# Optimization experiments

Measured on AMD Instinct MI355X. Metric: run time of the kernel, lower is better.

## Reference

```python
import jax, jax.numpy as jnp
import numpy as np

E = 2048   # embed_dim
H = 16     # num_heads
D = E // H # head_dim = 128
ROPE_BASE = 10000.0


def setup_inputs() -> dict:
    key = jax.random.key(0)
    ks = jax.random.split(key, 9)
    s = 0.02
    x = jax.random.normal(ks[0], (2, 2048, E), dtype=jnp.float32)
    Wq = jax.random.normal(ks[1], (E, E), dtype=jnp.float32) * s
    bq = jax.random.normal(ks[2], (E,), dtype=jnp.float32) * s
    Wk = jax.random.normal(ks[3], (E, E), dtype=jnp.float32) * s
    bk = jax.random.normal(ks[4], (E,), dtype=jnp.float32) * s
    Wv = jax.random.normal(ks[5], (E, E), dtype=jnp.float32) * s
    bv = jax.random.normal(ks[6], (E,), dtype=jnp.float32) * s
    Wo = jax.random.normal(ks[7], (E, E), dtype=jnp.float32) * s
    bo = jax.random.normal(ks[8], (E,), dtype=jnp.float32) * s
    return {"x": x, "Wq": Wq, "bq": bq, "Wk": Wk, "bk": bk,
            "Wv": Wv, "bv": bv, "Wo": Wo, "bo": bo}


def _rope_cos_sin(seq_len, dtype):
    inv_freq = 1.0 / (ROPE_BASE ** (jnp.arange(0, D, 2, dtype=jnp.float32) / D))
    pos = jnp.arange(seq_len, dtype=jnp.float32)
    freqs = pos[:, None] * inv_freq[None, :]          # (S, D/2)
    emb = jnp.concatenate([freqs, freqs], axis=-1)    # (S, D)
    return jnp.cos(emb).astype(dtype), jnp.sin(emb).astype(dtype)


def _rotate_half(t):
    t1, t2 = jnp.split(t, 2, axis=-1)
    return jnp.concatenate([-t2, t1], axis=-1)


def reference(x, Wq, bq, Wk, bk, Wv, bv, Wo, bo):
    B, S, _ = x.shape
    # QKV projections (torch Linear: x @ W.T + b)
    q = (x @ Wq.T + bq).reshape(B, S, H, D).transpose(0, 2, 1, 3)  # (B,H,S,D)
    k = (x @ Wk.T + bk).reshape(B, S, H, D).transpose(0, 2, 1, 3)
    v = (x @ Wv.T + bv).reshape(B, S, H, D).transpose(0, 2, 1, 3)
    # RoPE
    cos, sin = _rope_cos_sin(S, x.dtype)              # (S, D) each
    q = q * cos + _rotate_half(q) * sin
    k = k * cos + _rotate_half(k) * sin
    # Causal scaled dot-product attention
    scale = 1.0 / jnp.sqrt(jnp.asarray(D, dtype=x.dtype))
    scores = jnp.einsum('bhqd,bhkd->bhqk', q, k) * scale
    causal = jnp.tril(jnp.ones((S, S), dtype=bool))
    scores = jnp.where(causal, scores, jnp.asarray(-jnp.inf, dtype=x.dtype))
    attn = jax.nn.softmax(scores, axis=-1)
    out = jnp.einsum('bhqk,bhkd->bhqd', attn, v)      # (B,H,S,D)
    out = out.transpose(0, 2, 1, 3).reshape(B, S, E)
    return out @ Wo.T + bo
```

## Files before the change

kernel.cpp:

```cpp
#include <hip/hip_runtime.h>
#include <math.h>

typedef __bf16 bf16;
typedef __attribute__((ext_vector_type(2))) __bf16 bf16x2;
typedef __attribute__((ext_vector_type(4))) __bf16 bf16x4;
typedef __attribute__((ext_vector_type(8))) __bf16 bf16x8;
typedef __attribute__((ext_vector_type(4))) float f32x4;

#define GLD16(g, l) __builtin_amdgcn_global_load_lds( \
    (const __attribute__((address_space(1))) void*)(g), \
    (__attribute__((address_space(3))) void*)(l), 16, 0, 0)


__global__ void cast_bf16_kernel(const float* __restrict__ in, bf16* __restrict__ out, int n4) {
  int i = blockIdx.x * blockDim.x + threadIdx.x;
  if (i >= n4) return;
  float4 f = ((const float4*)in)[i];
  bf16x4 o;
  o[0] = (bf16)f.x; o[1] = (bf16)f.y; o[2] = (bf16)f.z; o[3] = (bf16)f.w;
  ((bf16x4*)out)[i] = o;
}

__global__ void bias_cat_kernel(const float* __restrict__ bq, const float* __restrict__ bk,
                                const float* __restrict__ bv, float* __restrict__ out) {
  int i = blockIdx.x * blockDim.x + threadIdx.x;
  if (i >= 6144) return;
  out[i] = (i < 2048) ? bq[i] : (i < 4096 ? bk[i - 2048] : bv[i - 4096]);
}

__global__ void rope_table_kernel(float* __restrict__ cost, float* __restrict__ sint) {
  int i = blockIdx.x * blockDim.x + threadIdx.x;
  int s = i >> 6, d = i & 63;
  float inv = powf(10000.0f, -(float)d / 64.0f);
  float ang = (float)s * inv;
  cost[i] = cosf(ang);
  sint[i] = sinf(ang);
}

__global__ void rope_transpose_kernel(const bf16* __restrict__ qkv,
                                      const float* __restrict__ cost, const float* __restrict__ sint,
                                      bf16* __restrict__ qr, bf16* __restrict__ kr, bf16* __restrict__ vr) {
  int idx = blockIdx.x * blockDim.x + threadIdx.x;
  int d = idx & 127;
  int h = (idx >> 7) & 15;
  int s = (idx >> 11) & 2047;
  int b = idx >> 22;
  const bf16* row = qkv + (size_t)(b * 2048 + s) * 6144;
  float c  = cost[(s << 6) | (d & 63)];
  float sn = sint[(s << 6) | (d & 63)];
  float qv = (float)row[(h << 7) | d];
  float qp = (float)row[(h << 7) | (d ^ 64)];
  float kv = (float)row[2048 + ((h << 7) | d)];
  float kp = (float)row[2048 + ((h << 7) | (d ^ 64))];
  float vv = (float)row[4096 + ((h << 7) | d)];
  float qrot = (d < 64) ? -qp : qp;
  float krot = (d < 64) ? -kp : kp;
  size_t o = ((size_t)((b << 4) | h) * 2048 + s) * 128 + d;
  qr[o] = (bf16)(qv * c + qrot * sn);
  kr[o] = (bf16)(kv * c + krot * sn);
  vr[o] = (bf16)vv;
}

__global__ void transpose_v_kernel(const bf16* __restrict__ vr, bf16* __restrict__ vt) {
  __shared__ bf16 Vl[64 * 72];
  const int bh = blockIdx.z;
  const int st = blockIdx.y;
  const int dt = blockIdx.x;
  const bf16* src = vr + ((size_t)bh * 2048 + st * 64) * 128 + dt * 64;
  bf16* dst = vt + ((size_t)bh * 128 + dt * 64) * 2048 + st * 64;
  const int t = threadIdx.x;
#pragma unroll
  for (int i = 0; i < 2; ++i) {
    int c = i * 256 + t;
    int r = c >> 3, c0 = (c & 7) * 8;
    *(bf16x8*)&Vl[r * 72 + c0] = *(const bf16x8*)&src[(size_t)r * 128 + c0];
  }
  __syncthreads();
#pragma unroll
  for (int i = 0; i < 2; ++i) {
    int c = i * 256 + t;
    int r = c >> 3, c0 = (c & 7) * 8;
    bf16x8 v;
#pragma unroll
    for (int j = 0; j < 8; ++j) v[j] = Vl[(c0 + j) * 72 + r];
    *(bf16x8*)&dst[(size_t)r * 2048 + c0] = v;
  }
}

template<bool OUT_BF16>
__global__ __launch_bounds__(256)
void gemm_bt_kernel(const bf16* __restrict__ A, const bf16* __restrict__ B,
                    const float* __restrict__ bias, void* __restrict__ Cp,
                    int M, int N, int K) {
  __shared__ bf16 Al[128 * 32];
  __shared__ bf16 Bl[128 * 32];
  const int t = threadIdx.x;
  const int wid = t >> 6, lane = t & 63;
  const int wr = wid >> 1, wc = wid & 1;
  const int lr = lane & 15, lk = lane >> 4;
  const int tm = blockIdx.y, tn = blockIdx.x;
  const bf16* Ab = A + (size_t)tm * 128 * K;
  const bf16* Bb = B + (size_t)tn * 128 * K;
  f32x4 acc[4][4] = {};
  for (int k0 = 0; k0 < K; k0 += 32) {
    __syncthreads();
#pragma unroll
    for (int c = 0; c < 2; ++c) {
      int e = (c * 256 + t) * 8;
      int row = e >> 5, kk = e & 31;
      GLD16(Ab + (size_t)row * K + k0 + kk, &Al[e]);
      GLD16(Bb + (size_t)row * K + k0 + kk, &Bl[e]);
    }
    __syncthreads();
    bf16x8 af[4], bf[4];
#pragma unroll
    for (int m = 0; m < 4; ++m) af[m] = *(const bf16x8*)&Al[(wr * 64 + m * 16 + lr) * 32 + lk * 8];
#pragma unroll
    for (int n = 0; n < 4; ++n) bf[n] = *(const bf16x8*)&Bl[(wc * 64 + n * 16 + lr) * 32 + lk * 8];
#pragma unroll
    for (int m = 0; m < 4; ++m)
#pragma unroll
      for (int n = 0; n < 4; ++n)
        acc[m][n] = __builtin_amdgcn_mfma_f32_16x16x32_bf16(af[m], bf[n], acc[m][n], 0, 0, 0);
  }
  const int rb = tm * 128 + wr * 64, cb = tn * 128 + wc * 64;
#pragma unroll
  for (int n = 0; n < 4; ++n) {
    int col = cb + n * 16 + lr;
    float bvl = bias[col];
#pragma unroll
    for (int m = 0; m < 4; ++m) {
#pragma unroll
      for (int r = 0; r < 4; ++r) {
        int row = rb + m * 16 + lk * 4 + r;
        float v = acc[m][n][r] + bvl;
        if (OUT_BF16) ((bf16*)Cp)[(size_t)row * N + col] = (bf16)v;
        else          ((float*)Cp)[(size_t)row * N + col] = v;
      }
    }
  }
}

template<bool OUT_BF16>
__global__ __launch_bounds__(512, 2)
void gemm256_kernel(const bf16* __restrict__ A, const bf16* __restrict__ B,
                    const float* __restrict__ bias, void* __restrict__ Cp,
                    int M, int N, int K) {
  __shared__ bf16 Al[2][2][128 * 64];
  __shared__ bf16 Bl[2][2][128 * 64];
  const int t = threadIdx.x;
  const int wid = t >> 6, lane = t & 63;
  const int wr = wid >> 2, wc = wid & 3;
  const int lr = lane & 15, lk = lane >> 4;
  const int tm = blockIdx.y, tn = blockIdx.x;
  const bf16* Ab = A + (size_t)tm * 256 * K;
  const bf16* Bb = B + (size_t)tn * 256 * K;
  const int NT = K >> 6;

  auto stageA = [&](int bp, int h, int kt) {
#pragma unroll
    for (int q = 0; q < 2; ++q) {
      int e = q * 512 + t;
      int r = e >> 3, c = e & 7;
      GLD16(Ab + (size_t)(h * 128 + r) * K + kt * 64 + ((c ^ (r & 7)) << 3), &Al[bp][h][e * 8]);
    }
  };
  auto stageB = [&](int bp, int h, int kt) {
#pragma unroll
    for (int q = 0; q < 2; ++q) {
      int e = q * 512 + t;
      int r = e >> 3, c = e & 7;
      GLD16(Bb + (size_t)(h * 128 + r) * K + kt * 64 + ((c ^ (r & 7)) << 3), &Bl[bp][h][e * 8]);
    }
  };

  f32x4 acc[8][4] = {};

  stageB(0, 0, 0); stageB(0, 1, 0);
  stageA(0, 0, 0); stageA(0, 1, 0);
  if (NT > 1) { stageB(1, 0, 1); stageB(1, 1, 1); }
  asm volatile("s_waitcnt vmcnt(4)" ::: "memory");
  __builtin_amdgcn_s_barrier();
  __builtin_amdgcn_sched_barrier(0);

  for (int u = 0; u < NT; ++u) {
    const int p = u & 1;
    const bf16* Ah = Al[p][wr];
    const bf16* Bh = Bl[p][wc >> 1];
    const int rb0 = (wc & 1) * 64;
    bf16x8 bfr[4][2];
#pragma unroll
    for (int j = 0; j < 4; ++j) {
      bf16x8 afr[2][2];
      if (j == 0) {
#pragma unroll
        for (int n = 0; n < 4; ++n)
#pragma unroll
          for (int kk = 0; kk < 2; ++kk) {
            int r = rb0 + n * 16 + lr;
            bfr[n][kk] = *(const bf16x8*)&Bh[r * 64 + ((((kk << 2) | lk) ^ (r & 7)) << 3)];
          }
      }
#pragma unroll
      for (int m2 = 0; m2 < 2; ++m2)
#pragma unroll
        for (int kk = 0; kk < 2; ++kk) {
          int r = (2 * j + m2) * 16 + lr;
          afr[m2][kk] = *(const bf16x8*)&Ah[r * 64 + ((((kk << 2) | lk) ^ (r & 7)) << 3)];
        }
      if (j == 0)      { if (u + 1 < NT) stageA(p ^ 1, 0, u + 1); }
      else if (j == 1) { if (u + 1 < NT) stageA(p ^ 1, 1, u + 1); }
      else if (j == 2) { if (u + 2 < NT) stageB(p, 0, u + 2); }
      else             { if (u + 2 < NT) stageB(p, 1, u + 2); }
      __builtin_amdgcn_s_barrier();
      asm volatile("s_waitcnt lgkmcnt(0)" ::: "memory");
      __builtin_amdgcn_sched_barrier(0);
      __builtin_amdgcn_s_setprio(1);
#pragma unroll
      for (int m2 = 0; m2 < 2; ++m2)
#pragma unroll
        for (int n = 0; n < 4; ++n)
#pragma unroll
          for (int kk = 0; kk < 2; ++kk)
            acc[2 * j + m2][n] = __builtin_amdgcn_mfma_f32_16x16x32_bf16(
                afr[m2][kk], bfr[n][kk], acc[2 * j + m2][n], 0, 0, 0);
      __builtin_amdgcn_s_setprio(0);
      __builtin_amdgcn_sched_barrier(0);
      if (j == 3) {
        if (u + 2 < NT) { asm volatile("s_waitcnt vmcnt(4)" ::: "memory"); }
        else            { asm volatile("s_waitcnt vmcnt(0)" ::: "memory"); }
      }
      __builtin_amdgcn_s_barrier();
      __builtin_amdgcn_sched_barrier(0);
    }
  }

  const int rb = tm * 256 + wr * 128, cb = tn * 256 + wc * 64;
#pragma unroll
  for (int n = 0; n < 4; ++n) {
    int col = cb + n * 16 + lr;
    float bvl = bias[col];
#pragma unroll
    for (int m = 0; m < 8; ++m) {
#pragma unroll
      for (int r = 0; r < 4; ++r) {
        int row = rb + m * 16 + lk * 4 + r;
        float v = acc[m][n][r] + bvl;
        if (OUT_BF16) ((bf16*)Cp)[(size_t)row * N + col] = (bf16)v;
        else          ((float*)Cp)[(size_t)row * N + col] = v;
      }
    }
  }
}

__global__ __launch_bounds__(256, 2)
void attn_kernel(const bf16* __restrict__ Q, const bf16* __restrict__ Kc,
                 const bf16* __restrict__ Vtg, bf16* __restrict__ O, int S) {
  __shared__ bf16 Kl[2][64 * 128];
  __shared__ bf16 Vt[2][128 * 64];
  __shared__ bf16 Pl[4][16 * 64];
  const int t = threadIdx.x, wid = t >> 6, lane = t & 63;
  const int lr = lane & 15, lk = lane >> 4;
  const int bh = blockIdx.y;
  const int NQ = S >> 6;
  const int qtA = blockIdx.x, qtB = NQ - 1 - qtA;
  const int ntA = qtA + 1, ntB = qtB + 1, total = ntA + ntB;
  const bf16* Qb = Q + (size_t)bh * S * 128;
  const bf16* Kb = Kc + (size_t)bh * S * 128;
  const bf16* Vb = Vtg + (size_t)bh * 128 * S;
  const int b = bh >> 4, h = bh & 15;
  const float scale = 0.08838834764831845f;

  bf16x8 qf[4];
  auto loadQ = [&](int q0) {
    int qrow = q0 + wid * 16 + lr;
#pragma unroll
    for (int kb = 0; kb < 4; ++kb)
      qf[kb] = *(const bf16x8*)&Qb[(size_t)qrow * 128 + kb * 32 + lk * 8];
  };
  auto stage = [&](int buf, int kv0) {
#pragma unroll
    for (int c = 0; c < 4; ++c) {
      int fc = c * 256 + t;
      int kvr = fc >> 4, cc = fc & 15;
      GLD16(Kb + (size_t)(kv0 + kvr) * 128 + (cc ^ (kvr & 7)) * 8, &Kl[buf][fc * 8]);
      int dr = fc >> 3, c2 = fc & 7;
      GLD16(Vb + (size_t)dr * S + kv0 + (c2 ^ (dr & 7)) * 8, &Vt[buf][fc * 8]);
    }
  };

  f32x4 o[8] = {};
  float mrun[4], lrun[4];
#pragma unroll
  for (int r = 0; r < 4; ++r) { mrun[r] = -INFINITY; lrun[r] = 0.f; }

  loadQ(qtA * 64);
  stage(0, 0);
  __syncthreads();
  int cur = 0;
  for (int ti = 0; ti < total; ++ti) {
    if (ti + 1 < total) {
      int tn = ti + 1;
      stage(cur ^ 1, ((tn < ntA) ? tn : tn - ntA) * 64);
    }
    __builtin_amdgcn_sched_barrier(0);
    const bool isA = ti < ntA;
    const int tt = isA ? ti : ti - ntA;
    const int nt = isA ? ntA : ntB;
    const int q0 = (isA ? qtA : qtB) * 64;
    const int kv0 = tt * 64;
    f32x4 sa[4];
    __builtin_amdgcn_s_setprio(1);
#pragma unroll
    for (int n = 0; n < 4; ++n) {
      sa[n] = (f32x4){0.f, 0.f, 0.f, 0.f};
      int kvl = n * 16 + lr;
#pragma unroll
      for (int kb = 0; kb < 4; ++kb) {
        bf16x8 kf = *(const bf16x8*)&Kl[cur][kvl * 128 + (((kb << 2) | lk) ^ (kvl & 7)) * 8];
        sa[n] = __builtin_amdgcn_mfma_f32_16x16x32_bf16(qf[kb], kf, sa[n], 0, 0, 0);
      }
    }
    __builtin_amdgcn_s_setprio(0);
    float p[4][4];
    float tmax[4] = {-INFINITY, -INFINITY, -INFINITY, -INFINITY};
    const bool lastTile = (tt == nt - 1);
#pragma unroll
    for (int n = 0; n < 4; ++n)
#pragma unroll
      for (int r = 0; r < 4; ++r) {
        float s = sa[n][r] * scale;
        if (lastTile) {
          int kvg = kv0 + n * 16 + lr;
          int qg = q0 + wid * 16 + lk * 4 + r;
          if (kvg > qg) s = -INFINITY;
        }
        p[n][r] = s;
        tmax[r] = fmaxf(tmax[r], s);
      }
#pragma unroll
    for (int r = 0; r < 4; ++r)
#pragma unroll
      for (int off = 1; off < 16; off <<= 1)
        tmax[r] = fmaxf(tmax[r], __shfl_xor(tmax[r], off));
    float alpha[4], rsum[4];
#pragma unroll
    for (int r = 0; r < 4; ++r) {
      float mnew = fmaxf(mrun[r], tmax[r]);
      alpha[r] = __expf(mrun[r] - mnew);
      mrun[r] = mnew;
      rsum[r] = 0.f;
#pragma unroll
      for (int n = 0; n < 4; ++n) {
        p[n][r] = __expf(p[n][r] - mnew);
        rsum[r] += p[n][r];
      }
    }
#pragma unroll
    for (int r = 0; r < 4; ++r) {
#pragma unroll
      for (int off = 1; off < 16; off <<= 1)
        rsum[r] += __shfl_xor(rsum[r], off);
      lrun[r] = lrun[r] * alpha[r] + rsum[r];
    }
#pragma unroll
    for (int n8 = 0; n8 < 8; ++n8)
#pragma unroll
      for (int r = 0; r < 4; ++r)
        o[n8][r] *= alpha[r];
#pragma unroll
    for (int n = 0; n < 4; ++n)
#pragma unroll
      for (int r = 0; r < 4; ++r) {
        int row = lk * 4 + r, col = n * 16 + lr;
        Pl[wid][(row * 64 + col) ^ ((row & 7) << 3)] = (bf16)p[n][r];
      }
    __builtin_amdgcn_s_setprio(1);
#pragma unroll
    for (int kb2 = 0; kb2 < 2; ++kb2) {
      bf16x8 pf = *(const bf16x8*)&Pl[wid][(lr * 64 + kb2 * 32 + lk * 8) ^ ((lr & 7) << 3)];
#pragma unroll
      for (int n8 = 0; n8 < 8; ++n8) {
        int dcol = n8 * 16 + lr;
        bf16x8 vf = *(const bf16x8*)&Vt[cur][(dcol * 64 + kb2 * 32 + lk * 8) ^ ((dcol & 7) << 3)];
        o[n8] = __builtin_amdgcn_mfma_f32_16x16x32_bf16(pf, vf, o[n8], 0, 0, 0);
      }
    }
    __builtin_amdgcn_s_setprio(0);
    if (ti == ntA - 1) {
#pragma unroll
      for (int r = 0; r < 4; ++r) {
        float rl = 1.0f / lrun[r];
        int row = qtA * 64 + wid * 16 + lk * 4 + r;
        size_t base = ((size_t)(b * S + row)) * 2048 + h * 128;
#pragma unroll
        for (int n8 = 0; n8 < 8; ++n8)
          O[base + n8 * 16 + lr] = (bf16)(o[n8][r] * rl);
      }
#pragma unroll
      for (int n8 = 0; n8 < 8; ++n8) o[n8] = (f32x4){0.f, 0.f, 0.f, 0.f};
#pragma unroll
      for (int r = 0; r < 4; ++r) { mrun[r] = -INFINITY; lrun[r] = 0.f; }
      loadQ(qtB * 64);
    }
    __syncthreads();
    cur ^= 1;
  }
#pragma unroll
  for (int r = 0; r < 4; ++r) {
    float rl = 1.0f / lrun[r];
    int row = qtB * 64 + wid * 16 + lk * 4 + r;
    size_t base = ((size_t)(b * S + row)) * 2048 + h * 128;
#pragma unroll
    for (int n8 = 0; n8 < 8; ++n8)
      O[base + n8 * 16 + lr] = (bf16)(o[n8][r] * rl);
  }
}


extern "C" void kernel_launch(void* const* d_in, const int* in_sizes, int n_in,
                              void* d_out, int out_size, void* d_ws, size_t ws_size,
                              hipStream_t stream) {
  const float* x  = (const float*)d_in[0];
  const float* Wq = (const float*)d_in[1];
  const float* bq = (const float*)d_in[2];
  const float* Wk = (const float*)d_in[3];
  const float* bk = (const float*)d_in[4];
  const float* Wv = (const float*)d_in[5];
  const float* bv = (const float*)d_in[6];
  const float* Wo = (const float*)d_in[7];
  const float* bo = (const float*)d_in[8];

  char* ws = (char*)d_ws;
  bf16* xb     = (bf16*)(ws);
  bf16* wqkv   = (bf16*)(ws + 16777216);
  bf16* wob    = (bf16*)(ws + 41943040);
  bf16* qkv    = (bf16*)(ws + 50331648);
  bf16* kr     = (bf16*)(ws + 100663296);
  bf16* vr     = (bf16*)(ws + 117440512);
  float* biasq = (float*)(ws + 134217728);
  float* cost  = (float*)(ws + 134242304);
  float* sint  = (float*)(ws + 134766592);
  bf16* qr = xb;
  bf16* attn_out = qkv;
  bf16* vt = (bf16*)(ws + 67108864);

  cast_bf16_kernel<<<8192, 256, 0, stream>>>(x, xb, 2097152);
  cast_bf16_kernel<<<4096, 256, 0, stream>>>(Wq, wqkv, 1048576);
  cast_bf16_kernel<<<4096, 256, 0, stream>>>(Wk, wqkv + 2048 * 2048, 1048576);
  cast_bf16_kernel<<<4096, 256, 0, stream>>>(Wv, wqkv + 2 * 2048 * 2048, 1048576);
  cast_bf16_kernel<<<4096, 256, 0, stream>>>(Wo, wob, 1048576);
  bias_cat_kernel<<<24, 256, 0, stream>>>(bq, bk, bv, biasq);
  rope_table_kernel<<<512, 256, 0, stream>>>(cost, sint);
  gemm256_kernel<true><<<dim3(24, 16), 512, 0, stream>>>(xb, wqkv, biasq, qkv, 4096, 6144, 2048);
  rope_transpose_kernel<<<32768, 256, 0, stream>>>(qkv, cost, sint, qr, kr, vr);
  transpose_v_kernel<<<dim3(2, 32, 32), 256, 0, stream>>>(vr, vt);
  attn_kernel<<<dim3(16, 32), 256, 0, stream>>>(qr, kr, vt, attn_out, 2048);
  gemm_bt_kernel<false><<<dim3(16, 32), 256, 0, stream>>>(attn_out, wob, bo, (float*)d_out, 4096, 2048, 2048);
}
```

Before: 329.3 us.

## Fuse prep kernels, apply Q RoPE in attention, retile GEMMs with swizzled blocks

The five cast kernels, the bias concat and the RoPE table are merged into a single launch. Q RoPE moves into the attention kernel's Q load, and K RoPE becomes a vectorized kernel that writes K only. The V transpose now reads straight from the qkv buffer, so the intermediate qr/vr copies disappear. The pipelined 256-row GEMM is parameterized by N tile width (192 for QKV, 128 for the output projection), replacing the simple 128x128 output GEMM, and both use XCD-style block index remapping for cache locality. Risks are fewer blocks and lower occupancy in the output GEMM, plus the extra RoPE work attention now does per Q tile.

```diff
diff --git a/kernel.cpp b/kernel.cpp
--- a/kernel.cpp
+++ b/kernel.cpp
@@ -11,69 +11,90 @@
     (const __attribute__((address_space(1))) void*)(g), \
     (__attribute__((address_space(3))) void*)(l), 16, 0, 0)
 
-
-__global__ void cast_bf16_kernel(const float* __restrict__ in, bf16* __restrict__ out, int n4) {
-  int i = blockIdx.x * blockDim.x + threadIdx.x;
-  if (i >= n4) return;
-  float4 f = ((const float4*)in)[i];
-  bf16x4 o;
-  o[0] = (bf16)f.x; o[1] = (bf16)f.y; o[2] = (bf16)f.z; o[3] = (bf16)f.w;
-  ((bf16x4*)out)[i] = o;
-}
-
-__global__ void bias_cat_kernel(const float* __restrict__ bq, const float* __restrict__ bk,
-                                const float* __restrict__ bv, float* __restrict__ out) {
-  int i = blockIdx.x * blockDim.x + threadIdx.x;
-  if (i >= 6144) return;
-  out[i] = (i < 2048) ? bq[i] : (i < 4096 ? bk[i - 2048] : bv[i - 4096]);
-}
-
-__global__ void rope_table_kernel(float* __restrict__ cost, float* __restrict__ sint) {
-  int i = blockIdx.x * blockDim.x + threadIdx.x;
-  int s = i >> 6, d = i & 63;
-  float inv = powf(10000.0f, -(float)d / 64.0f);
-  float ang = (float)s * inv;
-  cost[i] = cosf(ang);
-  sint[i] = sinf(ang);
-}
-
-__global__ void rope_transpose_kernel(const bf16* __restrict__ qkv,
-                                      const float* __restrict__ cost, const float* __restrict__ sint,
-                                      bf16* __restrict__ qr, bf16* __restrict__ kr, bf16* __restrict__ vr) {
+template<int N> __device__ __forceinline__ void wait_vm() {
+  static_assert(N == 0 || N == 2 || N == 3 || N == 4, "");
+  if constexpr (N == 0) asm volatile("s_waitcnt vmcnt(0)" ::: "memory");
+  else if constexpr (N == 2) asm volatile("s_waitcnt vmcnt(2)" ::: "memory");
+  else if constexpr (N == 3) asm volatile("s_waitcnt vmcnt(3)" ::: "memory");
+  else asm volatile("s_waitcnt vmcnt(4)" ::: "memory");
+}
+
+__global__ void prep_kernel(const float* __restrict__ x,
+                            const float* __restrict__ Wq, const float* __restrict__ Wk,
+                            const float* __restrict__ Wv, const float* __restrict__ Wo,
+                            const float* __restrict__ bq, const float* __restrict__ bk,
+                            const float* __restrict__ bv,
+                            bf16* __restrict__ xb, bf16* __restrict__ wqkv, bf16* __restrict__ wob,
+                            float* __restrict__ biasq, float* __restrict__ cost, float* __restrict__ sint) {
+  const int bid = blockIdx.x, t = threadIdx.x;
+  if (bid < 24576) {
+    const float* src;
+    bf16* dst;
+    int i;
+    if (bid < 8192)       { src = x;  dst = xb;                    i = bid * 256 + t; }
+    else if (bid < 12288) { src = Wq; dst = wqkv;                  i = (bid - 8192) * 256 + t; }
+    else if (bid < 16384) { src = Wk; dst = wqkv + 2048 * 2048;    i = (bid - 12288) * 256 + t; }
+    else if (bid < 20480) { src = Wv; dst = wqkv + 2 * 2048 * 2048; i = (bid - 16384) * 256 + t; }
+    else                  { src = Wo; dst = wob;                   i = (bid - 20480) * 256 + t; }
+    float4 f = ((const float4*)src)[i];
+    bf16x4 o;
+    o[0] = (bf16)f.x; o[1] = (bf16)f.y; o[2] = (bf16)f.z; o[3] = (bf16)f.w;
+    ((bf16x4*)dst)[i] = o;
+  } else if (bid < 25088) {
+    int i = (bid - 24576) * 256 + t;
+    int s = i >> 6, d = i & 63;
+    float inv = powf(10000.0f, -(float)d / 64.0f);
+    float ang = (float)s * inv;
+    cost[i] = cosf(ang);
+    sint[i] = sinf(ang);
+  } else {
+    int i = (bid - 25088) * 256 + t;
+    biasq[i] = (i < 2048) ? bq[i] : (i < 4096 ? bk[i - 2048] : bv[i - 4096]);
+  }
+}
+
+__global__ void rope_k_kernel(const bf16* __restrict__ qkv,
+                              const float* __restrict__ cost, const float* __restrict__ sint,
+                              bf16* __restrict__ kr) {
   int idx = blockIdx.x * blockDim.x + threadIdx.x;
-  int d = idx & 127;
-  int h = (idx >> 7) & 15;
-  int s = (idx >> 11) & 2047;
-  int b = idx >> 22;
-  const bf16* row = qkv + (size_t)(b * 2048 + s) * 6144;
-  float c  = cost[(s << 6) | (d & 63)];
-  float sn = sint[(s << 6) | (d & 63)];
-  float qv = (float)row[(h << 7) | d];
-  float qp = (float)row[(h << 7) | (d ^ 64)];
-  float kv = (float)row[2048 + ((h << 7) | d)];
-  float kp = (float)row[2048 + ((h << 7) | (d ^ 64))];
-  float vv = (float)row[4096 + ((h << 7) | d)];
-  float qrot = (d < 64) ? -qp : qp;
-  float krot = (d < 64) ? -kp : kp;
-  size_t o = ((size_t)((b << 4) | h) * 2048 + s) * 128 + d;
-  qr[o] = (bf16)(qv * c + qrot * sn);
-  kr[o] = (bf16)(kv * c + krot * sn);
-  vr[o] = (bf16)vv;
-}
-
-__global__ void transpose_v_kernel(const bf16* __restrict__ vr, bf16* __restrict__ vt) {
+  int dp = idx & 15;
+  int h = (idx >> 4) & 15;
+  int s = (idx >> 8) & 2047;
+  int b = idx >> 19;
+  int d0 = dp * 4;
+  const bf16* row = qkv + ((size_t)(b * 2048 + s) * 6144) + 2048 + h * 128;
+  bf16x4 klo = *(const bf16x4*)&row[d0];
+  bf16x4 khi = *(const bf16x4*)&row[d0 + 64];
+  float4 c4 = *(const float4*)&cost[(s << 6) + d0];
+  float4 s4 = *(const float4*)&sint[(s << 6) + d0];
+  float cf[4] = {c4.x, c4.y, c4.z, c4.w};
+  float sf[4] = {s4.x, s4.y, s4.z, s4.w};
+  bf16x4 olo, ohi;
+#pragma unroll
+  for (int j = 0; j < 4; ++j) {
+    float kl = (float)klo[j], kh = (float)khi[j];
+    olo[j] = (bf16)(kl * cf[j] - kh * sf[j]);
+    ohi[j] = (bf16)(kh * cf[j] + kl * sf[j]);
+  }
+  bf16* orow = kr + (((size_t)(b * 16 + h) * 2048 + s) * 128);
+  *(bf16x4*)&orow[d0] = olo;
+  *(bf16x4*)&orow[d0 + 64] = ohi;
+}
+
+__global__ void transpose_v_kernel(const bf16* __restrict__ qkv, bf16* __restrict__ vt) {
   __shared__ bf16 Vl[64 * 72];
   const int bh = blockIdx.z;
   const int st = blockIdx.y;
   const int dt = blockIdx.x;
-  const bf16* src = vr + ((size_t)bh * 2048 + st * 64) * 128 + dt * 64;
+  const int b = bh >> 4, h = bh & 15;
+  const bf16* src = qkv + ((size_t)(b * 2048 + st * 64) * 6144) + 4096 + h * 128 + dt * 64;
   bf16* dst = vt + ((size_t)bh * 128 + dt * 64) * 2048 + st * 64;
   const int t = threadIdx.x;
 #pragma unroll
   for (int i = 0; i < 2; ++i) {
     int c = i * 256 + t;
     int r = c >> 3, c0 = (c & 7) * 8;
-    *(bf16x8*)&Vl[r * 72 + c0] = *(const bf16x8*)&src[(size_t)r * 128 + c0];
+    *(bf16x8*)&Vl[r * 72 + c0] = *(const bf16x8*)&src[(size_t)r * 6144 + c0];
   }
   __syncthreads();
 #pragma unroll
@@ -87,74 +108,25 @@
   }
 }
 
-template<bool OUT_BF16>
-__global__ __launch_bounds__(256)
-void gemm_bt_kernel(const bf16* __restrict__ A, const bf16* __restrict__ B,
-                    const float* __restrict__ bias, void* __restrict__ Cp,
-                    int M, int N, int K) {
-  __shared__ bf16 Al[128 * 32];
-  __shared__ bf16 Bl[128 * 32];
-  const int t = threadIdx.x;
-  const int wid = t >> 6, lane = t & 63;
-  const int wr = wid >> 1, wc = wid & 1;
-  const int lr = lane & 15, lk = lane >> 4;
-  const int tm = blockIdx.y, tn = blockIdx.x;
-  const bf16* Ab = A + (size_t)tm * 128 * K;
-  const bf16* Bb = B + (size_t)tn * 128 * K;
-  f32x4 acc[4][4] = {};
-  for (int k0 = 0; k0 < K; k0 += 32) {
-    __syncthreads();
-#pragma unroll
-    for (int c = 0; c < 2; ++c) {
-      int e = (c * 256 + t) * 8;
-      int row = e >> 5, kk = e & 31;
-      GLD16(Ab + (size_t)row * K + k0 + kk, &Al[e]);
-      GLD16(Bb + (size_t)row * K + k0 + kk, &Bl[e]);
-    }
-    __syncthreads();
-    bf16x8 af[4], bf[4];
-#pragma unroll
-    for (int m = 0; m < 4; ++m) af[m] = *(const bf16x8*)&Al[(wr * 64 + m * 16 + lr) * 32 + lk * 8];
-#pragma unroll
-    for (int n = 0; n < 4; ++n) bf[n] = *(const bf16x8*)&Bl[(wc * 64 + n * 16 + lr) * 32 + lk * 8];
-#pragma unroll
-    for (int m = 0; m < 4; ++m)
-#pragma unroll
-      for (int n = 0; n < 4; ++n)
-        acc[m][n] = __builtin_amdgcn_mfma_f32_16x16x32_bf16(af[m], bf[n], acc[m][n], 0, 0, 0);
-  }
-  const int rb = tm * 128 + wr * 64, cb = tn * 128 + wc * 64;
-#pragma unroll
-  for (int n = 0; n < 4; ++n) {
-    int col = cb + n * 16 + lr;
-    float bvl = bias[col];
-#pragma unroll
-    for (int m = 0; m < 4; ++m) {
-#pragma unroll
-      for (int r = 0; r < 4; ++r) {
-        int row = rb + m * 16 + lk * 4 + r;
-        float v = acc[m][n][r] + bvl;
-        if (OUT_BF16) ((bf16*)Cp)[(size_t)row * N + col] = (bf16)v;
-        else          ((float*)Cp)[(size_t)row * N + col] = v;
-      }
-    }
-  }
-}
-
-template<bool OUT_BF16>
+template<int BN, bool OUT_BF16, int LOGNX>
 __global__ __launch_bounds__(512, 2)
 void gemm256_kernel(const bf16* __restrict__ A, const bf16* __restrict__ B,
                     const float* __restrict__ bias, void* __restrict__ Cp,
                     int M, int N, int K) {
+  constexpr int NB = BN / 64;
   __shared__ bf16 Al[2][2][128 * 64];
-  __shared__ bf16 Bl[2][2][128 * 64];
+  __shared__ bf16 Bl[2][NB][64 * 64];
   const int t = threadIdx.x;
   const int wid = t >> 6, lane = t & 63;
   const int wr = wid >> 2, wc = wid & 3;
   const int lr = lane & 15, lk = lane >> 4;
-  const int tm = blockIdx.y, tn = blockIdx.x;
+  const int nwg = (int)(gridDim.x * gridDim.y);
+  const int flat = (int)(blockIdx.y * gridDim.x + blockIdx.x);
+  const int fs = (flat & 7) * (nwg >> 3) + (flat >> 3);
+  const int tn = fs & ((1 << LOGNX) - 1);
+  const int tm = fs >> LOGNX;
   const bf16* Ab = A + (size_t)tm * 256 * K;
-  const bf16* Bb = B + (size_t)tn * 256 * K;
+  const bf16* Bb = B + (size_t)tn * BN * K;
   const int NT = K >> 6;
 
   auto stageA = [&](int bp, int h, int kt) {
@@ -165,40 +137,40 @@
       GLD16(Ab + (size_t)(h * 128 + r) * K + kt * 64 + ((c ^ (r & 7)) << 3), &Al[bp][h][e * 8]);
     }
   };
-  auto stageB = [&](int bp, int h, int kt) {
-#pragma unroll
-    for (int q = 0; q < 2; ++q) {
-      int e = q * 512 + t;
-      int r = e >> 3, c = e & 7;
-      GLD16(Bb + (size_t)(h * 128 + r) * K + kt * 64 + ((c ^ (r & 7)) << 3), &Bl[bp][h][e * 8]);
-    }
+  auto stageB = [&](int bp, int unit, int kt) {
+    int r = t >> 3, c = t & 7;
+    GLD16(Bb + (size_t)(unit * 64 + r) * K + kt * 64 + ((c ^ (r & 7)) << 3), &Bl[bp][unit][t * 8]);
   };
 
-  f32x4 acc[8][4] = {};
-
-  stageB(0, 0, 0); stageB(0, 1, 0);
+  f32x4 acc[8][NB] = {};
+
+#pragma unroll
+  for (int un = 0; un < NB; ++un) stageB(0, un, 0);
   stageA(0, 0, 0); stageA(0, 1, 0);
-  if (NT > 1) { stageB(1, 0, 1); stageB(1, 1, 1); }
-  asm volatile("s_waitcnt vmcnt(4)" ::: "memory");
+  if (NT > 1) {
+#pragma unroll
+    for (int un = 0; un < NB; ++un) stageB(1, un, 1);
+    wait_vm<NB>();
+  } else {
+    wait_vm<0>();
+  }
   __builtin_amdgcn_s_barrier();
   __builtin_amdgcn_sched_barrier(0);
 
   for (int u = 0; u < NT; ++u) {
     const int p = u & 1;
     const bf16* Ah = Al[p][wr];
-    const bf16* Bh = Bl[p][wc >> 1];
-    const int rb0 = (wc & 1) * 64;
-    bf16x8 bfr[4][2];
+    bf16x8 bfr[NB][2];
 #pragma unroll
     for (int j = 0; j < 4; ++j) {
       bf16x8 afr[2][2];
       if (j == 0) {
 #pragma unroll
-        for (int n = 0; n < 4; ++n)
+        for (int n = 0; n < NB; ++n)
 #pragma unroll
           for (int kk = 0; kk < 2; ++kk) {
-            int r = rb0 + n * 16 + lr;
-            bfr[n][kk] = *(const bf16x8*)&Bh[r * 64 + ((((kk << 2) | lk) ^ (r & 7)) << 3)];
+            int rb = wc * (NB * 16) + n * 16 + lr;
+            bfr[n][kk] = *(const bf16x8*)&Bl[p][rb >> 6][(rb & 63) * 64 + ((((kk << 2) | lk) ^ (rb & 7)) << 3)];
           }
       }
 #pragma unroll
@@ -210,8 +182,17 @@
         }
       if (j == 0)      { if (u + 1 < NT) stageA(p ^ 1, 0, u + 1); }
       else if (j == 1) { if (u + 1 < NT) stageA(p ^ 1, 1, u + 1); }
-      else if (j == 2) { if (u + 2 < NT) stageB(p, 0, u + 2); }
-      else             { if (u + 2 < NT) stageB(p, 1, u + 2); }
+      else if (j == 2) {
+        if (u + 2 < NT) {
+#pragma unroll
+          for (int un = 0; un < NB / 2; ++un) stageB(p, un, u + 2);
+        }
+      } else {
+        if (u + 2 < NT) {
+#pragma unroll
+          for (int un = NB / 2; un < NB; ++un) stageB(p, un, u + 2);
+        }
+      }
       __builtin_amdgcn_s_barrier();
       asm volatile("s_waitcnt lgkmcnt(0)" ::: "memory");
       __builtin_amdgcn_sched_barrier(0);
@@ -219,7 +200,7 @@
 #pragma unroll
       for (int m2 = 0; m2 < 2; ++m2)
 #pragma unroll
-        for (int n = 0; n < 4; ++n)
+        for (int n = 0; n < NB; ++n)
 #pragma unroll
           for (int kk = 0; kk < 2; ++kk)
             acc[2 * j + m2][n] = __builtin_amdgcn_mfma_f32_16x16x32_bf16(
@@ -227,17 +208,17 @@
       __builtin_amdgcn_s_setprio(0);
       __builtin_amdgcn_sched_barrier(0);
       if (j == 3) {
-        if (u + 2 < NT) { asm volatile("s_waitcnt vmcnt(4)" ::: "memory"); }
-        else            { asm volatile("s_waitcnt vmcnt(0)" ::: "memory"); }
+        if (u + 2 < NT) { wait_vm<NB>(); }
+        else            { wait_vm<0>(); }
       }
       __builtin_amdgcn_s_barrier();
       __builtin_amdgcn_sched_barrier(0);
     }
   }
 
-  const int rb = tm * 256 + wr * 128, cb = tn * 256 + wc * 64;
-#pragma unroll
-  for (int n = 0; n < 4; ++n) {
+  const int rb = tm * 256 + wr * 128, cb = tn * BN + wc * (NB * 16);
+#pragma unroll
+  for (int n = 0; n < NB; ++n) {
     int col = cb + n * 16 + lr;
     float bvl = bias[col];
 #pragma unroll
@@ -254,29 +235,42 @@
 }
 
 __global__ __launch_bounds__(256, 2)
-void attn_kernel(const bf16* __restrict__ Q, const bf16* __restrict__ Kc,
-                 const bf16* __restrict__ Vtg, bf16* __restrict__ O, int S) {
+void attn_kernel(const bf16* __restrict__ qkv, const bf16* __restrict__ Kc,
+                 const bf16* __restrict__ Vtg, const float* __restrict__ cost,
+                 const float* __restrict__ sint, bf16* __restrict__ O, int S) {
   __shared__ bf16 Kl[2][64 * 128];
   __shared__ bf16 Vt[2][128 * 64];
   __shared__ bf16 Pl[4][16 * 64];
   const int t = threadIdx.x, wid = t >> 6, lane = t & 63;
   const int lr = lane & 15, lk = lane >> 4;
   const int bh = blockIdx.y;
+  const int b = bh >> 4, h = bh & 15;
   const int NQ = S >> 6;
   const int qtA = blockIdx.x, qtB = NQ - 1 - qtA;
   const int ntA = qtA + 1, ntB = qtB + 1, total = ntA + ntB;
-  const bf16* Qb = Q + (size_t)bh * S * 128;
   const bf16* Kb = Kc + (size_t)bh * S * 128;
   const bf16* Vb = Vtg + (size_t)bh * 128 * S;
-  const int b = bh >> 4, h = bh & 15;
   const float scale = 0.08838834764831845f;
 
   bf16x8 qf[4];
   auto loadQ = [&](int q0) {
     int qrow = q0 + wid * 16 + lr;
-#pragma unroll
-    for (int kb = 0; kb < 4; ++kb)
-      qf[kb] = *(const bf16x8*)&Qb[(size_t)qrow * 128 + kb * 32 + lk * 8];
+    const bf16* qp = qkv + (size_t)(b * 2048 + qrow) * 6144 + h * 128;
+    bf16x8 raw[4];
+#pragma unroll
+    for (int kb = 0; kb < 4; ++kb) raw[kb] = *(const bf16x8*)&qp[kb * 32 + lk * 8];
+#pragma unroll
+    for (int kb = 0; kb < 4; ++kb) {
+      const float* cb = cost + (qrow << 6) + ((kb & 1) << 5) + lk * 8;
+      const float* sb = sint + (qrow << 6) + ((kb & 1) << 5) + lk * 8;
+#pragma unroll
+      for (int j = 0; j < 8; ++j) {
+        float qv = (float)raw[kb][j];
+        float qo = (float)raw[kb ^ 2][j];
+        float rot = (kb < 2) ? -qo : qo;
+        qf[kb][j] = (bf16)(qv * cb[j] + rot * sb[j]);
+      }
+    }
   };
   auto stage = [&](int buf, int kv0) {
 #pragma unroll
@@ -437,24 +431,17 @@
   bf16* wob    = (bf16*)(ws + 41943040);
   bf16* qkv    = (bf16*)(ws + 50331648);
   bf16* kr     = (bf16*)(ws + 100663296);
-  bf16* vr     = (bf16*)(ws + 117440512);
+  bf16* vt     = (bf16*)(ws + 117440512);
   float* biasq = (float*)(ws + 134217728);
   float* cost  = (float*)(ws + 134242304);
   float* sint  = (float*)(ws + 134766592);
-  bf16* qr = xb;
-  bf16* attn_out = qkv;
-  bf16* vt = (bf16*)(ws + 67108864);
-
-  cast_bf16_kernel<<<8192, 256, 0, stream>>>(x, xb, 2097152);
-  cast_bf16_kernel<<<4096, 256, 0, stream>>>(Wq, wqkv, 1048576);
-  cast_bf16_kernel<<<4096, 256, 0, stream>>>(Wk, wqkv + 2048 * 2048, 1048576);
-  cast_bf16_kernel<<<4096, 256, 0, stream>>>(Wv, wqkv + 2 * 2048 * 2048, 1048576);
-  cast_bf16_kernel<<<4096, 256, 0, stream>>>(Wo, wob, 1048576);
-  bias_cat_kernel<<<24, 256, 0, stream>>>(bq, bk, bv, biasq);
-  rope_table_kernel<<<512, 256, 0, stream>>>(cost, sint);
-  gemm256_kernel<true><<<dim3(24, 16), 512, 0, stream>>>(xb, wqkv, biasq, qkv, 4096, 6144, 2048);
-  rope_transpose_kernel<<<32768, 256, 0, stream>>>(qkv, cost, sint, qr, kr, vr);
-  transpose_v_kernel<<<dim3(2, 32, 32), 256, 0, stream>>>(vr, vt);
-  attn_kernel<<<dim3(16, 32), 256, 0, stream>>>(qr, kr, vt, attn_out, 2048);
-  gemm_bt_kernel<false><<<dim3(16, 32), 256, 0, stream>>>(attn_out, wob, bo, (float*)d_out, 4096, 2048, 2048);
-}
+  bf16* attn_out = xb;
+
+  prep_kernel<<<25112, 256, 0, stream>>>(x, Wq, Wk, Wv, Wo, bq, bk, bv,
+                                         xb, wqkv, wob, biasq, cost, sint);
+  gemm256_kernel<192, true, 5><<<dim3(32, 16), 512, 0, stream>>>(xb, wqkv, biasq, qkv, 4096, 6144, 2048);
+  rope_k_kernel<<<4096, 256, 0, stream>>>(qkv, cost, sint, kr);
+  transpose_v_kernel<<<dim3(2, 32, 32), 256, 0, stream>>>(qkv, vt);
+  attn_kernel<<<dim3(16, 32), 256, 0, stream>>>(qkv, kr, vt, cost, sint, attn_out, 2048);
+  gemm256_kernel<128, false, 4><<<dim3(16, 16), 512, 0, stream>>>(attn_out, wob, bo, (float*)d_out, 4096, 2048, 2048);
+}
```

Result: faster. 299.2 us (-9.2%).
